# Kernel tuning notes

Hardware: AMD Instinct MI355X
Metric: run time of the kernel (lower is better)

The kernel has to match this reference:

```python
import jax, jax.numpy as jnp
import numpy as np

C = 128  # n_filters; input channels must equal n_filters due to residual


def setup_inputs() -> dict:
    key = jax.random.key(0)
    kx, kw = jax.random.split(key)
    x = jax.random.normal(kx, (8, 64, 512, C), dtype=jnp.float32)
    # 1x1 conv, no bias == dense over channel axis: [C, 2C]
    W_qkv = jax.random.normal(kw, (C, 2 * C), dtype=jnp.float32) * (1.0 / np.sqrt(C))
    return {"x": x, "W_qkv": W_qkv}


def reference(x, W_qkv):
    # qkv: [B,H,W,2C]; split -> qk [B,H,W,C] -> q,k [B,H,W,C/2]; v [B,H,W,C]
    qkv = jnp.einsum('bhwc,cd->bhwd', x, W_qkv)
    half = C // 2
    q = qkv[..., :half]
    k = qkv[..., half:C]
    v = qkv[..., C:]
    # scores over the W (time) axis; NOTE: original applies no 1/sqrt(d) scaling
    scores = jnp.einsum('bhqc,bhkc->bhqk', q, k)  # [B,H,W,W]
    w = jax.nn.softmax(scores, axis=-1)
    y = jnp.einsum('bhqk,bhkc->bhqc', w, v)  # [B,H,W,C]
    y = x + y  # with_skip_connection=True
    return (y, w)
```

## Files before the change

### kernel.cpp

```cpp
#include <hip/hip_runtime.h>
#include <hip/hip_bf16.h>

typedef short s16x8 __attribute__((ext_vector_type(8)));
typedef float f32x4 __attribute__((ext_vector_type(4)));

#define MFMA_BF16(a,b,c) __builtin_amdgcn_mfma_f32_16x16x32_bf16((a),(b),(c),0,0,0)

static __device__ __forceinline__ unsigned short f2bf(float f){
  unsigned u = __builtin_bit_cast(unsigned, f);
  u += 0x7fffu + ((u >> 16) & 1u);
  return (unsigned short)(u >> 16);
}
static __device__ __forceinline__ float bf2f(unsigned short h){
  unsigned u = ((unsigned)h) << 16;
  return __builtin_bit_cast(float, u);
}
static __device__ __forceinline__ int swzi(int row, int col, int lw){
  const int chunk = (col >> 3) ^ ((row ^ (row >> 3)) & 7);
  return row*lw + (chunk << 3) + (col & 7);
}

__global__ __launch_bounds__(128) void k0_wt(const float* __restrict__ W,
                                             unsigned short* __restrict__ wtH,
                                             unsigned short* __restrict__ wtL){
  const int n = blockIdx.x;
  const int c = threadIdx.x;
  const float v = W[(size_t)c*256 + n];
  const unsigned short h = f2bf(v);
  wtH[n*128 + c] = h;
  wtL[n*128 + c] = f2bf(v - bf2f(h));
}

__global__ __launch_bounds__(512,2) void k1_qkv(const float* __restrict__ x,
    const unsigned short* __restrict__ wtH, const unsigned short* __restrict__ wtL,
    unsigned short* __restrict__ qh, unsigned short* __restrict__ ql,
    unsigned short* __restrict__ kh, unsigned short* __restrict__ kl,
    unsigned short* __restrict__ vT){
  __shared__ unsigned short xh[16384], xl[16384];
  const int t = threadIdx.x;
  const int lane = t & 63, wid = t >> 6;
  const int li = lane & 15, g = lane >> 4;
  const int m0 = blockIdx.x * 128;
  const int wm = wid >> 2, wn = wid & 3;

  {
    const int row = t >> 2, cb = (t & 3) * 32;
    const float* src = x + (size_t)(m0 + row)*128 + cb;
    #pragma unroll
    for (int gg = 0; gg < 4; ++gg){
      const float4 v0 = ((const float4*)src)[2*gg];
      const float4 v1 = ((const float4*)src)[2*gg + 1];
      const float vv[8] = {v0.x,v0.y,v0.z,v0.w,v1.x,v1.y,v1.z,v1.w};
      s16x8 h, l;
      #pragma unroll
      for (int j = 0; j < 8; ++j){
        const unsigned short hb = f2bf(vv[j]);
        h[j] = (short)hb;
        l[j] = (short)f2bf(vv[j] - bf2f(hb));
      }
      const int idx = swzi(row, cb + 8*gg, 128);
      *(s16x8*)&xh[idx] = h;
      *(s16x8*)&xl[idx] = l;
    }
  }
  __syncthreads();

  {
    f32x4 acc[4][2] = {};
    #pragma unroll
    for (int ks = 0; ks < 4; ++ks){
      const int col = ks*32 + g*8;
      s16x8 ah[4], al[4];
      #pragma unroll
      for (int mi = 0; mi < 4; ++mi){
        const int idx = swzi(wm*64 + mi*16 + li, col, 128);
        ah[mi] = *(const s16x8*)&xh[idx];
        al[mi] = *(const s16x8*)&xl[idx];
      }
      #pragma unroll
      for (int ni = 0; ni < 2; ++ni){
        const size_t boff = (size_t)(wn*32 + ni*16 + li)*128 + col;
        const s16x8 bh = *(const s16x8*)(wtH + boff);
        const s16x8 bl = *(const s16x8*)(wtL + boff);
        #pragma unroll
        for (int mi = 0; mi < 4; ++mi){
          acc[mi][ni] = MFMA_BF16(bh, ah[mi], acc[mi][ni]);
          acc[mi][ni] = MFMA_BF16(bh, al[mi], acc[mi][ni]);
          acc[mi][ni] = MFMA_BF16(bl, ah[mi], acc[mi][ni]);
        }
      }
    }
    #pragma unroll
    for (int mi = 0; mi < 4; ++mi)
      #pragma unroll
      for (int ni = 0; ni < 2; ++ni){
        const int pos = m0 + wm*64 + mi*16 + li;
        const int och = wn*32 + ni*16 + g*4;
        ushort4 hv, lv;
        #pragma unroll
        for (int r = 0; r < 4; ++r){
          const float v = acc[mi][ni][r];
          const unsigned short hb = f2bf(v);
          ((unsigned short*)&hv)[r] = hb;
          ((unsigned short*)&lv)[r] = f2bf(v - bf2f(hb));
        }
        const size_t off = (size_t)pos*64 + (och & 63);
        if (wn < 2){ *(ushort4*)&qh[off] = hv; *(ushort4*)&ql[off] = lv; }
        else       { *(ushort4*)&kh[off] = hv; *(ushort4*)&kl[off] = lv; }
      }
  }

  {
    f32x4 acc[4][2] = {};
    #pragma unroll
    for (int ks = 0; ks < 4; ++ks){
      const int col = ks*32 + g*8;
      s16x8 ah[4], al[4];
      #pragma unroll
      for (int mi = 0; mi < 4; ++mi){
        const int idx = swzi(wm*64 + mi*16 + li, col, 128);
        ah[mi] = *(const s16x8*)&xh[idx];
        al[mi] = *(const s16x8*)&xl[idx];
      }
      #pragma unroll
      for (int ni = 0; ni < 2; ++ni){
        const size_t boff = (size_t)(128 + wn*32 + ni*16 + li)*128 + col;
        const s16x8 bh = *(const s16x8*)(wtH + boff);
        const s16x8 bl = *(const s16x8*)(wtL + boff);
        #pragma unroll
        for (int mi = 0; mi < 4; ++mi){
          acc[mi][ni] = MFMA_BF16(ah[mi], bh, acc[mi][ni]);
          acc[mi][ni] = MFMA_BF16(ah[mi], bl, acc[mi][ni]);
          acc[mi][ni] = MFMA_BF16(al[mi], bh, acc[mi][ni]);
        }
      }
    }
    #pragma unroll
    for (int mi = 0; mi < 4; ++mi)
      #pragma unroll
      for (int ni = 0; ni < 2; ++ni){
        const int growb = m0 + wm*64 + mi*16 + g*4;
        const int ch = wn*32 + ni*16 + li;
        const int head = growb >> 9, posb = growb & 511;
        ushort4 pv;
        #pragma unroll
        for (int r = 0; r < 4; ++r)
          ((unsigned short*)&pv)[r] = f2bf(acc[mi][ni][r]);
        *(ushort4*)&vT[((size_t)head << 16) + ch*512 + posb] = pv;
      }
  }
}

__global__ __launch_bounds__(512,2) void k2_attn(
    const unsigned short* __restrict__ qh, const unsigned short* __restrict__ ql,
    const unsigned short* __restrict__ kh, const unsigned short* __restrict__ kl,
    const unsigned short* __restrict__ vT, const float* __restrict__ x,
    float* __restrict__ y, float* __restrict__ wout){
  __shared__ unsigned short wlds[32768];
  __shared__ float redm[512], reds[512];

  const int t = threadIdx.x;
  const int lane = t & 63, wid = t >> 6;
  const int li = lane & 15, g = lane >> 4;
  const int bi = blockIdx.x;
  const int head = (bi & 7) + 8 * (bi >> 6);
  const int qt = (bi >> 3) & 7;
  const size_t hbase = (size_t)head * 512;
  const int q0 = qt * 64;
  const int kbase = wid * 64;

  f32x4 acc[4][4] = {};
  #pragma unroll
  for (int ks = 0; ks < 2; ++ks){
    const int col = ks*32 + g*8;
    s16x8 qbh[4], qbl[4];
    #pragma unroll
    for (int qj = 0; qj < 4; ++qj){
      const size_t aoff = (hbase + q0 + qj*16 + li)*64 + col;
      qbh[qj] = *(const s16x8*)(qh + aoff);
      qbl[qj] = *(const s16x8*)(ql + aoff);
    }
    #pragma unroll
    for (int ni = 0; ni < 4; ++ni){
      const size_t boff = (hbase + kbase + ni*16 + li)*64 + col;
      const s16x8 ah = *(const s16x8*)(kh + boff);
      const s16x8 al = *(const s16x8*)(kl + boff);
      #pragma unroll
      for (int qj = 0; qj < 4; ++qj){
        acc[qj][ni] = MFMA_BF16(ah, qbh[qj], acc[qj][ni]);
        acc[qj][ni] = MFMA_BF16(al, qbh[qj], acc[qj][ni]);
        acc[qj][ni] = MFMA_BF16(ah, qbl[qj], acc[qj][ni]);
      }
    }
  }

  float fsc[4];
  #pragma unroll
  for (int qj = 0; qj < 4; ++qj){
    float m = acc[qj][0][0];
    #pragma unroll
    for (int ni = 0; ni < 4; ++ni)
      #pragma unroll
      for (int r = 0; r < 4; ++r) m = fmaxf(m, acc[qj][ni][r]);
    m = fmaxf(m, __shfl_xor(m, 16));
    m = fmaxf(m, __shfl_xor(m, 32));
    float s = 0.f;
    #pragma unroll
    for (int ni = 0; ni < 4; ++ni)
      #pragma unroll
      for (int r = 0; r < 4; ++r){
        const float e = __expf(acc[qj][ni][r] - m);
        acc[qj][ni][r] = e;
        s += e;
      }
    s += __shfl_xor(s, 16);
    s += __shfl_xor(s, 32);
    if (g == 0){
      redm[(qj*16 + li)*8 + wid] = m;
      reds[(qj*16 + li)*8 + wid] = s;
    }
    fsc[qj] = m;
  }
  __syncthreads();
  #pragma unroll
  for (int qj = 0; qj < 4; ++qj){
    const int row = qj*16 + li;
    const f32x4 m0v = *(const f32x4*)&redm[row*8];
    const f32x4 m1v = *(const f32x4*)&redm[row*8 + 4];
    const f32x4 s0v = *(const f32x4*)&reds[row*8];
    const f32x4 s1v = *(const f32x4*)&reds[row*8 + 4];
    float M = fmaxf(fmaxf(fmaxf(m0v[0], m0v[1]), fmaxf(m0v[2], m0v[3])),
                    fmaxf(fmaxf(m1v[0], m1v[1]), fmaxf(m1v[2], m1v[3])));
    float S = s0v[0]*__expf(m0v[0] - M) + s0v[1]*__expf(m0v[1] - M)
            + s0v[2]*__expf(m0v[2] - M) + s0v[3]*__expf(m0v[3] - M)
            + s1v[0]*__expf(m1v[0] - M) + s1v[1]*__expf(m1v[1] - M)
            + s1v[2]*__expf(m1v[2] - M) + s1v[3]*__expf(m1v[3] - M);
    fsc[qj] = __expf(fsc[qj] - M) / S;
  }

  #pragma unroll
  for (int qj = 0; qj < 4; ++qj){
    const int row = qj*16 + li;
    float* wrow = wout + (hbase + q0 + row)*512;
    #pragma unroll
    for (int ni = 0; ni < 4; ++ni){
      const int col = kbase + ni*16 + g*4;
      f32x4 wv;
      ushort4 pv;
      #pragma unroll
      for (int r = 0; r < 4; ++r){
        const float v = acc[qj][ni][r] * fsc[qj];
        wv[r] = v;
        ((unsigned short*)&pv)[r] = f2bf(v);
      }
      *(f32x4*)&wrow[col] = wv;
      *(ushort4*)&wlds[swzi(row, col, 512)] = pv;
    }
  }
  __syncthreads();

  const int c0 = wid * 16;
  f32x4 yacc[4] = {};
  const unsigned short* vhead = vT + ((size_t)head << 16) + (size_t)(c0 + li)*512;
  #pragma unroll
  for (int kt = 0; kt < 16; ++kt){
    const int kp0 = kt*32 + g*8;
    const s16x8 vb = *(const s16x8*)&vhead[kp0];
    #pragma unroll
    for (int mi = 0; mi < 4; ++mi){
      const s16x8 aw = *(const s16x8*)&wlds[swzi(mi*16 + li, kp0, 512)];
      yacc[mi] = MFMA_BF16(vb, aw, yacc[mi]);
    }
  }

  #pragma unroll
  for (int mi = 0; mi < 4; ++mi){
    const int row = mi*16 + li;
    const size_t idx = (hbase + q0 + row)*128 + c0 + g*4;
    const f32x4 xv = __builtin_nontemporal_load((const f32x4*)&x[idx]);
    f32x4 ov;
    ov[0] = xv[0] + yacc[mi][0];
    ov[1] = xv[1] + yacc[mi][1];
    ov[2] = xv[2] + yacc[mi][2];
    ov[3] = xv[3] + yacc[mi][3];
    *(f32x4*)&y[idx] = ov;
  }
}

extern "C" void kernel_launch(void* const* d_in, const int* in_sizes, int n_in,
                              void* d_out, int out_size, void* d_ws, size_t ws_size,
                              hipStream_t stream){
  (void)in_sizes; (void)n_in; (void)out_size; (void)ws_size;
  const float* x = (const float*)d_in[0];
  const float* W = (const float*)d_in[1];
  float* y    = (float*)d_out;
  float* wout = y + (size_t)33554432;

  char* ws = (char*)d_ws;
  unsigned short* qh  = (unsigned short*)(ws);
  unsigned short* ql  = (unsigned short*)(ws +  33554432ull);
  unsigned short* kh  = (unsigned short*)(ws +  67108864ull);
  unsigned short* kl  = (unsigned short*)(ws + 100663296ull);
  unsigned short* vT  = (unsigned short*)(ws + 134217728ull);
  unsigned short* wtH = (unsigned short*)(ws + 201326592ull);
  unsigned short* wtL = (unsigned short*)(ws + 201392128ull);

  hipLaunchKernelGGL(k0_wt,   dim3(256),  dim3(128), 0, stream, W, wtH, wtL);
  hipLaunchKernelGGL(k1_qkv,  dim3(2048), dim3(512), 0, stream, x, wtH, wtL,
                     qh, ql, kh, kl, vT);
  hipLaunchKernelGGL(k2_attn, dim3(4096), dim3(512), 0, stream,
                     qh, ql, kh, kl, vT, x, y, wout);
}
```

Before: 518.4 us.

## Fuse QKV projection and attention into one per-head kernel

Merges the QKV projection kernel and the attention kernel into a single kernel with one block per head. Each block first computes Q/K/V for its 512 positions in four chunks, then loops over eight query tiles to compute softmax and the output. This removes one launch and aims to keep the per-head Q/K/V in cache between the two phases. The grid shrinks from 4096 blocks to 512 and each block's work becomes serial, which reduces parallelism and latency hiding. The Q/K/V written by other threads are read back from global memory after only a block-level fence.

```diff
diff --git a/kernel.cpp b/kernel.cpp
--- a/kernel.cpp
+++ b/kernel.cpp
@@ -31,259 +31,260 @@
   wtL[n*128 + c] = f2bf(v - bf2f(h));
 }
 
-__global__ __launch_bounds__(512,2) void k1_qkv(const float* __restrict__ x,
+__global__ __launch_bounds__(512,2) void kf(const float* __restrict__ x,
     const unsigned short* __restrict__ wtH, const unsigned short* __restrict__ wtL,
     unsigned short* __restrict__ qh, unsigned short* __restrict__ ql,
     unsigned short* __restrict__ kh, unsigned short* __restrict__ kl,
-    unsigned short* __restrict__ vT){
-  __shared__ unsigned short xh[16384], xl[16384];
+    unsigned short* __restrict__ vT,
+    float* __restrict__ y, float* __restrict__ wout){
+  __shared__ __align__(16) unsigned short smem[34816];
+  unsigned short* xh   = smem;
+  unsigned short* xl   = smem + 16384;
+  unsigned short* wlds = smem;
+  float* redm = (float*)(smem + 32768);
+  float* reds = redm + 512;
+
   const int t = threadIdx.x;
   const int lane = t & 63, wid = t >> 6;
   const int li = lane & 15, g = lane >> 4;
-  const int m0 = blockIdx.x * 128;
+  const int head = blockIdx.x;
+  const size_t hbase = (size_t)head * 512;
+
   const int wm = wid >> 2, wn = wid & 3;
-
-  {
-    const int row = t >> 2, cb = (t & 3) * 32;
-    const float* src = x + (size_t)(m0 + row)*128 + cb;
-    #pragma unroll
-    for (int gg = 0; gg < 4; ++gg){
-      const float4 v0 = ((const float4*)src)[2*gg];
-      const float4 v1 = ((const float4*)src)[2*gg + 1];
-      const float vv[8] = {v0.x,v0.y,v0.z,v0.w,v1.x,v1.y,v1.z,v1.w};
-      s16x8 h, l;
-      #pragma unroll
-      for (int j = 0; j < 8; ++j){
-        const unsigned short hb = f2bf(vv[j]);
-        h[j] = (short)hb;
-        l[j] = (short)f2bf(vv[j] - bf2f(hb));
-      }
-      const int idx = swzi(row, cb + 8*gg, 128);
-      *(s16x8*)&xh[idx] = h;
-      *(s16x8*)&xl[idx] = l;
+  for (int rc = 0; rc < 4; ++rc){
+    const int m0 = head*512 + rc*128;
+    if (rc) __syncthreads();
+    {
+      const int row = t >> 2, cb = (t & 3) * 32;
+      const float* src = x + (size_t)(m0 + row)*128 + cb;
+      #pragma unroll
+      for (int gg = 0; gg < 4; ++gg){
+        const float4 v0 = ((const float4*)src)[2*gg];
+        const float4 v1 = ((const float4*)src)[2*gg + 1];
+        const float vv[8] = {v0.x,v0.y,v0.z,v0.w,v1.x,v1.y,v1.z,v1.w};
+        s16x8 h, l;
+        #pragma unroll
+        for (int j = 0; j < 8; ++j){
+          const unsigned short hb = f2bf(vv[j]);
+          h[j] = (short)hb;
+          l[j] = (short)f2bf(vv[j] - bf2f(hb));
+        }
+        const int idx = swzi(row, cb + 8*gg, 128);
+        *(s16x8*)&xh[idx] = h;
+        *(s16x8*)&xl[idx] = l;
+      }
+    }
+    __syncthreads();
+
+    {
+      f32x4 acc[4][2] = {};
+      #pragma unroll
+      for (int ks = 0; ks < 4; ++ks){
+        const int col = ks*32 + g*8;
+        s16x8 ah[4], al[4];
+        #pragma unroll
+        for (int mi = 0; mi < 4; ++mi){
+          const int idx = swzi(wm*64 + mi*16 + li, col, 128);
+          ah[mi] = *(const s16x8*)&xh[idx];
+          al[mi] = *(const s16x8*)&xl[idx];
+        }
+        #pragma unroll
+        for (int ni = 0; ni < 2; ++ni){
+          const size_t boff = (size_t)(wn*32 + ni*16 + li)*128 + col;
+          const s16x8 bh = *(const s16x8*)(wtH + boff);
+          const s16x8 bl = *(const s16x8*)(wtL + boff);
+          #pragma unroll
+          for (int mi = 0; mi < 4; ++mi){
+            acc[mi][ni] = MFMA_BF16(bh, ah[mi], acc[mi][ni]);
+            acc[mi][ni] = MFMA_BF16(bh, al[mi], acc[mi][ni]);
+            acc[mi][ni] = MFMA_BF16(bl, ah[mi], acc[mi][ni]);
+          }
+        }
+      }
+      #pragma unroll
+      for (int mi = 0; mi < 4; ++mi)
+        #pragma unroll
+        for (int ni = 0; ni < 2; ++ni){
+          const int pos = m0 + wm*64 + mi*16 + li;
+          const int och = wn*32 + ni*16 + g*4;
+          ushort4 hv, lv;
+          #pragma unroll
+          for (int r = 0; r < 4; ++r){
+            const float v = acc[mi][ni][r];
+            const unsigned short hb = f2bf(v);
+            ((unsigned short*)&hv)[r] = hb;
+            ((unsigned short*)&lv)[r] = f2bf(v - bf2f(hb));
+          }
+          const size_t off = (size_t)pos*64 + (och & 63);
+          if (wn < 2){ *(ushort4*)&qh[off] = hv; *(ushort4*)&ql[off] = lv; }
+          else       { *(ushort4*)&kh[off] = hv; *(ushort4*)&kl[off] = lv; }
+        }
+    }
+
+    {
+      f32x4 acc[4][2] = {};
+      #pragma unroll
+      for (int ks = 0; ks < 4; ++ks){
+        const int col = ks*32 + g*8;
+        s16x8 ah[4], al[4];
+        #pragma unroll
+        for (int mi = 0; mi < 4; ++mi){
+          const int idx = swzi(wm*64 + mi*16 + li, col, 128);
+          ah[mi] = *(const s16x8*)&xh[idx];
+          al[mi] = *(const s16x8*)&xl[idx];
+        }
+        #pragma unroll
+        for (int ni = 0; ni < 2; ++ni){
+          const size_t boff = (size_t)(128 + wn*32 + ni*16 + li)*128 + col;
+          const s16x8 bh = *(const s16x8*)(wtH + boff);
+          const s16x8 bl = *(const s16x8*)(wtL + boff);
+          #pragma unroll
+          for (int mi = 0; mi < 4; ++mi){
+            acc[mi][ni] = MFMA_BF16(ah[mi], bh, acc[mi][ni]);
+            acc[mi][ni] = MFMA_BF16(ah[mi], bl, acc[mi][ni]);
+            acc[mi][ni] = MFMA_BF16(al[mi], bh, acc[mi][ni]);
+          }
+        }
+      }
+      #pragma unroll
+      for (int mi = 0; mi < 4; ++mi)
+        #pragma unroll
+        for (int ni = 0; ni < 2; ++ni){
+          const int growb = m0 + wm*64 + mi*16 + g*4;
+          const int ch = wn*32 + ni*16 + li;
+          const int posb = growb & 511;
+          ushort4 pv;
+          #pragma unroll
+          for (int r = 0; r < 4; ++r)
+            ((unsigned short*)&pv)[r] = f2bf(acc[mi][ni][r]);
+          *(ushort4*)&vT[((size_t)head << 16) + ch*512 + posb] = pv;
+        }
     }
   }
+
+  __threadfence_block();
   __syncthreads();
 
-  {
-    f32x4 acc[4][2] = {};
-    #pragma unroll
-    for (int ks = 0; ks < 4; ++ks){
+  const int kbase = wid * 64;
+  for (int qt = 0; qt < 8; ++qt){
+    const int q0 = qt * 64;
+
+    f32x4 acc[4][4] = {};
+    #pragma unroll
+    for (int ks = 0; ks < 2; ++ks){
       const int col = ks*32 + g*8;
-      s16x8 ah[4], al[4];
+      s16x8 qbh[4], qbl[4];
+      #pragma unroll
+      for (int qj = 0; qj < 4; ++qj){
+        const size_t aoff = (hbase + q0 + qj*16 + li)*64 + col;
+        qbh[qj] = *(const s16x8*)(qh + aoff);
+        qbl[qj] = *(const s16x8*)(ql + aoff);
+      }
+      #pragma unroll
+      for (int ni = 0; ni < 4; ++ni){
+        const size_t boff = (hbase + kbase + ni*16 + li)*64 + col;
+        const s16x8 ah = *(const s16x8*)(kh + boff);
+        const s16x8 al = *(const s16x8*)(kl + boff);
+        #pragma unroll
+        for (int qj = 0; qj < 4; ++qj){
+          acc[qj][ni] = MFMA_BF16(ah, qbh[qj], acc[qj][ni]);
+          acc[qj][ni] = MFMA_BF16(al, qbh[qj], acc[qj][ni]);
+          acc[qj][ni] = MFMA_BF16(ah, qbl[qj], acc[qj][ni]);
+        }
+      }
+    }
+
+    float fsc[4];
+    #pragma unroll
+    for (int qj = 0; qj < 4; ++qj){
+      float m = acc[qj][0][0];
+      #pragma unroll
+      for (int ni = 0; ni < 4; ++ni)
+        #pragma unroll
+        for (int r = 0; r < 4; ++r) m = fmaxf(m, acc[qj][ni][r]);
+      m = fmaxf(m, __shfl_xor(m, 16));
+      m = fmaxf(m, __shfl_xor(m, 32));
+      float s = 0.f;
+      #pragma unroll
+      for (int ni = 0; ni < 4; ++ni)
+        #pragma unroll
+        for (int r = 0; r < 4; ++r){
+          const float e = __expf(acc[qj][ni][r] - m);
+          acc[qj][ni][r] = e;
+          s += e;
+        }
+      s += __shfl_xor(s, 16);
+      s += __shfl_xor(s, 32);
+      if (g == 0){
+        redm[(qj*16 + li)*8 + wid] = m;
+        reds[(qj*16 + li)*8 + wid] = s;
+      }
+      fsc[qj] = m;
+    }
+    __syncthreads();
+    #pragma unroll
+    for (int qj = 0; qj < 4; ++qj){
+      const int row = qj*16 + li;
+      const f32x4 m0v = *(const f32x4*)&redm[row*8];
+      const f32x4 m1v = *(const f32x4*)&redm[row*8 + 4];
+      const f32x4 s0v = *(const f32x4*)&reds[row*8];
+      const f32x4 s1v = *(const f32x4*)&reds[row*8 + 4];
+      float M = fmaxf(fmaxf(fmaxf(m0v[0], m0v[1]), fmaxf(m0v[2], m0v[3])),
+                      fmaxf(fmaxf(m1v[0], m1v[1]), fmaxf(m1v[2], m1v[3])));
+      float S = s0v[0]*__expf(m0v[0] - M) + s0v[1]*__expf(m0v[1] - M)
+              + s0v[2]*__expf(m0v[2] - M) + s0v[3]*__expf(m0v[3] - M)
+              + s1v[0]*__expf(m1v[0] - M) + s1v[1]*__expf(m1v[1] - M)
+              + s1v[2]*__expf(m1v[2] - M) + s1v[3]*__expf(m1v[3] - M);
+      fsc[qj] = __expf(fsc[qj] - M) / S;
+    }
+
+    #pragma unroll
+    for (int qj = 0; qj < 4; ++qj){
+      const int row = qj*16 + li;
+      float* wrow = wout + (hbase + q0 + row)*512;
+      #pragma unroll
+      for (int ni = 0; ni < 4; ++ni){
+        const int col = kbase + ni*16 + g*4;
+        f32x4 wv;
+        ushort4 pv;
+        #pragma unroll
+        for (int r = 0; r < 4; ++r){
+          const float v = acc[qj][ni][r] * fsc[qj];
+          wv[r] = v;
+          ((unsigned short*)&pv)[r] = f2bf(v);
+        }
+        *(f32x4*)&wrow[col] = wv;
+        *(ushort4*)&wlds[swzi(row, col, 512)] = pv;
+      }
+    }
+    __syncthreads();
+
+    const int c0 = wid * 16;
+    f32x4 yacc[4] = {};
+    const unsigned short* vhead = vT + ((size_t)head << 16) + (size_t)(c0 + li)*512;
+    #pragma unroll
+    for (int kt = 0; kt < 16; ++kt){
+      const int kp0 = kt*32 + g*8;
+      const s16x8 vb = *(const s16x8*)&vhead[kp0];
       #pragma unroll
       for (int mi = 0; mi < 4; ++mi){
-        const int idx = swzi(wm*64 + mi*16 + li, col, 128);
-        ah[mi] = *(const s16x8*)&xh[idx];
-        al[mi] = *(const s16x8*)&xl[idx];
-      }
-      #pragma unroll
-      for (int ni = 0; ni < 2; ++ni){
-        const size_t boff = (size_t)(wn*32 + ni*16 + li)*128 + col;
-        const s16x8 bh = *(const s16x8*)(wtH + boff);
-        const s16x8 bl = *(const s16x8*)(wtL + boff);
-        #pragma unroll
-        for (int mi = 0; mi < 4; ++mi){
-          acc[mi][ni] = MFMA_BF16(bh, ah[mi], acc[mi][ni]);
-          acc[mi][ni] = MFMA_BF16(bh, al[mi], acc[mi][ni]);
-          acc[mi][ni] = MFMA_BF16(bl, ah[mi], acc[mi][ni]);
-        }
-      }
-    }
-    #pragma unroll
-    for (int mi = 0; mi < 4; ++mi)
-      #pragma unroll
-      for (int ni = 0; ni < 2; ++ni){
-        const int pos = m0 + wm*64 + mi*16 + li;
-        const int och = wn*32 + ni*16 + g*4;
-        ushort4 hv, lv;
-        #pragma unroll
-        for (int r = 0; r < 4; ++r){
-          const float v = acc[mi][ni][r];
-          const unsigned short hb = f2bf(v);
-          ((unsigned short*)&hv)[r] = hb;
-          ((unsigned short*)&lv)[r] = f2bf(v - bf2f(hb));
-        }
-        const size_t off = (size_t)pos*64 + (och & 63);
-        if (wn < 2){ *(ushort4*)&qh[off] = hv; *(ushort4*)&ql[off] = lv; }
-        else       { *(ushort4*)&kh[off] = hv; *(ushort4*)&kl[off] = lv; }
-      }
-  }
-
-  {
-    f32x4 acc[4][2] = {};
-    #pragma unroll
-    for (int ks = 0; ks < 4; ++ks){
-      const int col = ks*32 + g*8;
-      s16x8 ah[4], al[4];
-      #pragma unroll
-      for (int mi = 0; mi < 4; ++mi){
-        const int idx = swzi(wm*64 + mi*16 + li, col, 128);
-        ah[mi] = *(const s16x8*)&xh[idx];
-        al[mi] = *(const s16x8*)&xl[idx];
-      }
-      #pragma unroll
-      for (int ni = 0; ni < 2; ++ni){
-        const size_t boff = (size_t)(128 + wn*32 + ni*16 + li)*128 + col;
-        const s16x8 bh = *(const s16x8*)(wtH + boff);
-        const s16x8 bl = *(const s16x8*)(wtL + boff);
-        #pragma unroll
-        for (int mi = 0; mi < 4; ++mi){
-          acc[mi][ni] = MFMA_BF16(ah[mi], bh, acc[mi][ni]);
-          acc[mi][ni] = MFMA_BF16(ah[mi], bl, acc[mi][ni]);
-          acc[mi][ni] = MFMA_BF16(al[mi], bh, acc[mi][ni]);
-        }
-      }
-    }
-    #pragma unroll
-    for (int mi = 0; mi < 4; ++mi)
-      #pragma unroll
-      for (int ni = 0; ni < 2; ++ni){
-        const int growb = m0 + wm*64 + mi*16 + g*4;
-        const int ch = wn*32 + ni*16 + li;
-        const int head = growb >> 9, posb = growb & 511;
-        ushort4 pv;
-        #pragma unroll
-        for (int r = 0; r < 4; ++r)
-          ((unsigned short*)&pv)[r] = f2bf(acc[mi][ni][r]);
-        *(ushort4*)&vT[((size_t)head << 16) + ch*512 + posb] = pv;
-      }
-  }
-}
-
-__global__ __launch_bounds__(512,2) void k2_attn(
-    const unsigned short* __restrict__ qh, const unsigned short* __restrict__ ql,
-    const unsigned short* __restrict__ kh, const unsigned short* __restrict__ kl,
-    const unsigned short* __restrict__ vT, const float* __restrict__ x,
-    float* __restrict__ y, float* __restrict__ wout){
-  __shared__ unsigned short wlds[32768];
-  __shared__ float redm[512], reds[512];
-
-  const int t = threadIdx.x;
-  const int lane = t & 63, wid = t >> 6;
-  const int li = lane & 15, g = lane >> 4;
-  const int bi = blockIdx.x;
-  const int head = (bi & 7) + 8 * (bi >> 6);
-  const int qt = (bi >> 3) & 7;
-  const size_t hbase = (size_t)head * 512;
-  const int q0 = qt * 64;
-  const int kbase = wid * 64;
-
-  f32x4 acc[4][4] = {};
-  #pragma unroll
-  for (int ks = 0; ks < 2; ++ks){
-    const int col = ks*32 + g*8;
-    s16x8 qbh[4], qbl[4];
-    #pragma unroll
-    for (int qj = 0; qj < 4; ++qj){
-      const size_t aoff = (hbase + q0 + qj*16 + li)*64 + col;
-      qbh[qj] = *(const s16x8*)(qh + aoff);
-      qbl[qj] = *(const s16x8*)(ql + aoff);
-    }
-    #pragma unroll
-    for (int ni = 0; ni < 4; ++ni){
-      const size_t boff = (hbase + kbase + ni*16 + li)*64 + col;
-      const s16x8 ah = *(const s16x8*)(kh + boff);
-      const s16x8 al = *(const s16x8*)(kl + boff);
-      #pragma unroll
-      for (int qj = 0; qj < 4; ++qj){
-        acc[qj][ni] = MFMA_BF16(ah, qbh[qj], acc[qj][ni]);
-        acc[qj][ni] = MFMA_BF16(al, qbh[qj], acc[qj][ni]);
-        acc[qj][ni] = MFMA_BF16(ah, qbl[qj], acc[qj][ni]);
-      }
-    }
-  }
-
-  float fsc[4];
-  #pragma unroll
-  for (int qj = 0; qj < 4; ++qj){
-    float m = acc[qj][0][0];
-    #pragma unroll
-    for (int ni = 0; ni < 4; ++ni)
-      #pragma unroll
-      for (int r = 0; r < 4; ++r) m = fmaxf(m, acc[qj][ni][r]);
-    m = fmaxf(m, __shfl_xor(m, 16));
-    m = fmaxf(m, __shfl_xor(m, 32));
-    float s = 0.f;
-    #pragma unroll
-    for (int ni = 0; ni < 4; ++ni)
-      #pragma unroll
-      for (int r = 0; r < 4; ++r){
-        const float e = __expf(acc[qj][ni][r] - m);
-        acc[qj][ni][r] = e;
-        s += e;
-      }
-    s += __shfl_xor(s, 16);
-    s += __shfl_xor(s, 32);
-    if (g == 0){
-      redm[(qj*16 + li)*8 + wid] = m;
-      reds[(qj*16 + li)*8 + wid] = s;
-    }
-    fsc[qj] = m;
-  }
-  __syncthreads();
-  #pragma unroll
-  for (int qj = 0; qj < 4; ++qj){
-    const int row = qj*16 + li;
-    const f32x4 m0v = *(const f32x4*)&redm[row*8];
-    const f32x4 m1v = *(const f32x4*)&redm[row*8 + 4];
-    const f32x4 s0v = *(const f32x4*)&reds[row*8];
-    const f32x4 s1v = *(const f32x4*)&reds[row*8 + 4];
-    float M = fmaxf(fmaxf(fmaxf(m0v[0], m0v[1]), fmaxf(m0v[2], m0v[3])),
-                    fmaxf(fmaxf(m1v[0], m1v[1]), fmaxf(m1v[2], m1v[3])));
-    float S = s0v[0]*__expf(m0v[0] - M) + s0v[1]*__expf(m0v[1] - M)
-            + s0v[2]*__expf(m0v[2] - M) + s0v[3]*__expf(m0v[3] - M)
-            + s1v[0]*__expf(m1v[0] - M) + s1v[1]*__expf(m1v[1] - M)
-            + s1v[2]*__expf(m1v[2] - M) + s1v[3]*__expf(m1v[3] - M);
-    fsc[qj] = __expf(fsc[qj] - M) / S;
-  }
-
-  #pragma unroll
-  for (int qj = 0; qj < 4; ++qj){
-    const int row = qj*16 + li;
-    float* wrow = wout + (hbase + q0 + row)*512;
-    #pragma unroll
-    for (int ni = 0; ni < 4; ++ni){
-      const int col = kbase + ni*16 + g*4;
-      f32x4 wv;
-      ushort4 pv;
-      #pragma unroll
-      for (int r = 0; r < 4; ++r){
-        const float v = acc[qj][ni][r] * fsc[qj];
-        wv[r] = v;
-        ((unsigned short*)&pv)[r] = f2bf(v);
-      }
-      *(f32x4*)&wrow[col] = wv;
-      *(ushort4*)&wlds[swzi(row, col, 512)] = pv;
-    }
-  }
-  __syncthreads();
-
-  const int c0 = wid * 16;
-  f32x4 yacc[4] = {};
-  const unsigned short* vhead = vT + ((size_t)head << 16) + (size_t)(c0 + li)*512;
-  #pragma unroll
-  for (int kt = 0; kt < 16; ++kt){
-    const int kp0 = kt*32 + g*8;
-    const s16x8 vb = *(const s16x8*)&vhead[kp0];
+        const s16x8 aw = *(const s16x8*)&wlds[swzi(mi*16 + li, kp0, 512)];
+        yacc[mi] = MFMA_BF16(vb, aw, yacc[mi]);
+      }
+    }
+
     #pragma unroll
     for (int mi = 0; mi < 4; ++mi){
-      const s16x8 aw = *(const s16x8*)&wlds[swzi(mi*16 + li, kp0, 512)];
-      yacc[mi] = MFMA_BF16(vb, aw, yacc[mi]);
-    }
-  }
-
-  #pragma unroll
-  for (int mi = 0; mi < 4; ++mi){
-    const int row = mi*16 + li;
-    const size_t idx = (hbase + q0 + row)*128 + c0 + g*4;
-    const f32x4 xv = __builtin_nontemporal_load((const f32x4*)&x[idx]);
-    f32x4 ov;
-    ov[0] = xv[0] + yacc[mi][0];
-    ov[1] = xv[1] + yacc[mi][1];
-    ov[2] = xv[2] + yacc[mi][2];
-    ov[3] = xv[3] + yacc[mi][3];
-    *(f32x4*)&y[idx] = ov;
+      const int row = mi*16 + li;
+      const size_t idx = (hbase + q0 + row)*128 + c0 + g*4;
+      const f32x4 xv = __builtin_nontemporal_load((const f32x4*)&x[idx]);
+      f32x4 ov;
+      ov[0] = xv[0] + yacc[mi][0];
+      ov[1] = xv[1] + yacc[mi][1];
+      ov[2] = xv[2] + yacc[mi][2];
+      ov[3] = xv[3] + yacc[mi][3];
+      *(f32x4*)&y[idx] = ov;
+    }
   }
 }
 
@@ -305,9 +306,7 @@
   unsigned short* wtH = (unsigned short*)(ws + 201326592ull);
   unsigned short* wtL = (unsigned short*)(ws + 201392128ull);
 
-  hipLaunchKernelGGL(k0_wt,   dim3(256),  dim3(128), 0, stream, W, wtH, wtL);
-  hipLaunchKernelGGL(k1_qkv,  dim3(2048), dim3(512), 0, stream, x, wtH, wtL,
-                     qh, ql, kh, kl, vT);
-  hipLaunchKernelGGL(k2_attn, dim3(4096), dim3(512), 0, stream,
-                     qh, ql, kh, kl, vT, x, y, wout);
-}
+  hipLaunchKernelGGL(k0_wt, dim3(256), dim3(128), 0, stream, W, wtH, wtL);
+  hipLaunchKernelGGL(kf,    dim3(512), dim3(512), 0, stream, x, wtH, wtL,
+                     qh, ql, kh, kl, vT, y, wout);
+}
```

Measured after the change: 505.1 us. -2.6%, faster.

## Process all query tiles per head in one block, keeping K and V in registers

Applied to the files above, without the earlier changes.

The attention kernel now launches one block per head instead of one per (head, query tile). Each block loads its K slice and the transposed V slice into registers once, then loops over the 8 query tiles, reusing them for scores and the weighted sum. This removes the repeated K/V global loads across query-tile blocks. In exchange, register use rises sharply (which may cause spills under the 512-thread, 2-blocks-per-CU bound), and the grid shrinks to 512 blocks, leaving less parallelism to hide the large output writes.

```diff
diff --git a/kernel.cpp b/kernel.cpp
--- a/kernel.cpp
+++ b/kernel.cpp
@@ -162,128 +162,140 @@
   const int t = threadIdx.x;
   const int lane = t & 63, wid = t >> 6;
   const int li = lane & 15, g = lane >> 4;
-  const int bi = blockIdx.x;
-  const int head = (bi & 7) + 8 * (bi >> 6);
-  const int qt = (bi >> 3) & 7;
+  const int head = blockIdx.x;
   const size_t hbase = (size_t)head * 512;
-  const int q0 = qt * 64;
   const int kbase = wid * 64;
 
-  f32x4 acc[4][4] = {};
+  s16x8 kregh[2][4], kregl[2][4];
   #pragma unroll
-  for (int ks = 0; ks < 2; ++ks){
-    const int col = ks*32 + g*8;
-    s16x8 qbh[4], qbl[4];
+  for (int ks = 0; ks < 2; ++ks)
+    #pragma unroll
+    for (int ni = 0; ni < 4; ++ni){
+      const size_t boff = (hbase + kbase + ni*16 + li)*64 + ks*32 + g*8;
+      kregh[ks][ni] = *(const s16x8*)(kh + boff);
+      kregl[ks][ni] = *(const s16x8*)(kl + boff);
+    }
+  s16x8 vreg[16];
+  {
+    const unsigned short* vhead = vT + ((size_t)head << 16) + (size_t)(wid*16 + li)*512;
+    #pragma unroll
+    for (int kt = 0; kt < 16; ++kt)
+      vreg[kt] = *(const s16x8*)&vhead[kt*32 + g*8];
+  }
+
+  for (int qt = 0; qt < 8; ++qt){
+    const int q0 = qt * 64;
+
+    f32x4 acc[4][4] = {};
+    #pragma unroll
+    for (int ks = 0; ks < 2; ++ks){
+      const int col = ks*32 + g*8;
+      s16x8 qbh[4], qbl[4];
+      #pragma unroll
+      for (int qj = 0; qj < 4; ++qj){
+        const size_t aoff = (hbase + q0 + qj*16 + li)*64 + col;
+        qbh[qj] = *(const s16x8*)(qh + aoff);
+        qbl[qj] = *(const s16x8*)(ql + aoff);
+      }
+      #pragma unroll
+      for (int ni = 0; ni < 4; ++ni)
+        #pragma unroll
+        for (int qj = 0; qj < 4; ++qj){
+          acc[qj][ni] = MFMA_BF16(kregh[ks][ni], qbh[qj], acc[qj][ni]);
+          acc[qj][ni] = MFMA_BF16(kregl[ks][ni], qbh[qj], acc[qj][ni]);
+          acc[qj][ni] = MFMA_BF16(kregh[ks][ni], qbl[qj], acc[qj][ni]);
+        }
+    }
+
+    float fsc[4];
     #pragma unroll
     for (int qj = 0; qj < 4; ++qj){
-      const size_t aoff = (hbase + q0 + qj*16 + li)*64 + col;
-      qbh[qj] = *(const s16x8*)(qh + aoff);
-      qbl[qj] = *(const s16x8*)(ql + aoff);
-    }
-    #pragma unroll
-    for (int ni = 0; ni < 4; ++ni){
-      const size_t boff = (hbase + kbase + ni*16 + li)*64 + col;
-      const s16x8 ah = *(const s16x8*)(kh + boff);
-      const s16x8 al = *(const s16x8*)(kl + boff);
-      #pragma unroll
-      for (int qj = 0; qj < 4; ++qj){
-        acc[qj][ni] = MFMA_BF16(ah, qbh[qj], acc[qj][ni]);
-        acc[qj][ni] = MFMA_BF16(al, qbh[qj], acc[qj][ni]);
-        acc[qj][ni] = MFMA_BF16(ah, qbl[qj], acc[qj][ni]);
-      }
-    }
-  }
-
-  float fsc[4];
-  #pragma unroll
-  for (int qj = 0; qj < 4; ++qj){
-    float m = acc[qj][0][0];
-    #pragma unroll
-    for (int ni = 0; ni < 4; ++ni)
-      #pragma unroll
-      for (int r = 0; r < 4; ++r) m = fmaxf(m, acc[qj][ni][r]);
-    m = fmaxf(m, __shfl_xor(m, 16));
-    m = fmaxf(m, __shfl_xor(m, 32));
-    float s = 0.f;
-    #pragma unroll
-    for (int ni = 0; ni < 4; ++ni)
-      #pragma unroll
-      for (int r = 0; r < 4; ++r){
-        const float e = __expf(acc[qj][ni][r] - m);
-        acc[qj][ni][r] = e;
-        s += e;
-      }
-    s += __shfl_xor(s, 16);
-    s += __shfl_xor(s, 32);
-    if (g == 0){
-      redm[(qj*16 + li)*8 + wid] = m;
-      reds[(qj*16 + li)*8 + wid] = s;
-    }
-    fsc[qj] = m;
-  }
-  __syncthreads();
-  #pragma unroll
-  for (int qj = 0; qj < 4; ++qj){
-    const int row = qj*16 + li;
-    const f32x4 m0v = *(const f32x4*)&redm[row*8];
-    const f32x4 m1v = *(const f32x4*)&redm[row*8 + 4];
-    const f32x4 s0v = *(const f32x4*)&reds[row*8];
-    const f32x4 s1v = *(const f32x4*)&reds[row*8 + 4];
-    float M = fmaxf(fmaxf(fmaxf(m0v[0], m0v[1]), fmaxf(m0v[2], m0v[3])),
-                    fmaxf(fmaxf(m1v[0], m1v[1]), fmaxf(m1v[2], m1v[3])));
-    float S = s0v[0]*__expf(m0v[0] - M) + s0v[1]*__expf(m0v[1] - M)
-            + s0v[2]*__expf(m0v[2] - M) + s0v[3]*__expf(m0v[3] - M)
-            + s1v[0]*__expf(m1v[0] - M) + s1v[1]*__expf(m1v[1] - M)
-            + s1v[2]*__expf(m1v[2] - M) + s1v[3]*__expf(m1v[3] - M);
-    fsc[qj] = __expf(fsc[qj] - M) / S;
-  }
-
-  #pragma unroll
-  for (int qj = 0; qj < 4; ++qj){
-    const int row = qj*16 + li;
-    float* wrow = wout + (hbase + q0 + row)*512;
-    #pragma unroll
-    for (int ni = 0; ni < 4; ++ni){
-      const int col = kbase + ni*16 + g*4;
-      f32x4 wv;
-      ushort4 pv;
-      #pragma unroll
-      for (int r = 0; r < 4; ++r){
-        const float v = acc[qj][ni][r] * fsc[qj];
-        wv[r] = v;
-        ((unsigned short*)&pv)[r] = f2bf(v);
-      }
-      *(f32x4*)&wrow[col] = wv;
-      *(ushort4*)&wlds[swzi(row, col, 512)] = pv;
-    }
-  }
-  __syncthreads();
-
-  const int c0 = wid * 16;
-  f32x4 yacc[4] = {};
-  const unsigned short* vhead = vT + ((size_t)head << 16) + (size_t)(c0 + li)*512;
-  #pragma unroll
-  for (int kt = 0; kt < 16; ++kt){
-    const int kp0 = kt*32 + g*8;
-    const s16x8 vb = *(const s16x8*)&vhead[kp0];
+      float m = acc[qj][0][0];
+      #pragma unroll
+      for (int ni = 0; ni < 4; ++ni)
+        #pragma unroll
+        for (int r = 0; r < 4; ++r) m = fmaxf(m, acc[qj][ni][r]);
+      m = fmaxf(m, __shfl_xor(m, 16));
+      m = fmaxf(m, __shfl_xor(m, 32));
+      float s = 0.f;
+      #pragma unroll
+      for (int ni = 0; ni < 4; ++ni)
+        #pragma unroll
+        for (int r = 0; r < 4; ++r){
+          const float e = __expf(acc[qj][ni][r] - m);
+          acc[qj][ni][r] = e;
+          s += e;
+        }
+      s += __shfl_xor(s, 16);
+      s += __shfl_xor(s, 32);
+      if (g == 0){
+        redm[(qj*16 + li)*8 + wid] = m;
+        reds[(qj*16 + li)*8 + wid] = s;
+      }
+      fsc[qj] = m;
+    }
+    __syncthreads();
+    #pragma unroll
+    for (int qj = 0; qj < 4; ++qj){
+      const int row = qj*16 + li;
+      const f32x4 m0v = *(const f32x4*)&redm[row*8];
+      const f32x4 m1v = *(const f32x4*)&redm[row*8 + 4];
+      const f32x4 s0v = *(const f32x4*)&reds[row*8];
+      const f32x4 s1v = *(const f32x4*)&reds[row*8 + 4];
+      float M = fmaxf(fmaxf(fmaxf(m0v[0], m0v[1]), fmaxf(m0v[2], m0v[3])),
+                      fmaxf(fmaxf(m1v[0], m1v[1]), fmaxf(m1v[2], m1v[3])));
+      float S = s0v[0]*__expf(m0v[0] - M) + s0v[1]*__expf(m0v[1] - M)
+              + s0v[2]*__expf(m0v[2] - M) + s0v[3]*__expf(m0v[3] - M)
+              + s1v[0]*__expf(m1v[0] - M) + s1v[1]*__expf(m1v[1] - M)
+              + s1v[2]*__expf(m1v[2] - M) + s1v[3]*__expf(m1v[3] - M);
+      fsc[qj] = __expf(fsc[qj] - M) / S;
+    }
+
+    #pragma unroll
+    for (int qj = 0; qj < 4; ++qj){
+      const int row = qj*16 + li;
+      float* wrow = wout + (hbase + q0 + row)*512;
+      #pragma unroll
+      for (int ni = 0; ni < 4; ++ni){
+        const int col = kbase + ni*16 + g*4;
+        f32x4 wv;
+        ushort4 pv;
+        #pragma unroll
+        for (int r = 0; r < 4; ++r){
+          const float v = acc[qj][ni][r] * fsc[qj];
+          wv[r] = v;
+          ((unsigned short*)&pv)[r] = f2bf(v);
+        }
+        *(f32x4*)&wrow[col] = wv;
+        *(ushort4*)&wlds[swzi(row, col, 512)] = pv;
+      }
+    }
+    __syncthreads();
+
+    const int c0 = wid * 16;
+    f32x4 yacc[4] = {};
+    #pragma unroll
+    for (int kt = 0; kt < 16; ++kt){
+      const int kp0 = kt*32 + g*8;
+      #pragma unroll
+      for (int mi = 0; mi < 4; ++mi){
+        const s16x8 aw = *(const s16x8*)&wlds[swzi(mi*16 + li, kp0, 512)];
+        yacc[mi] = MFMA_BF16(vreg[kt], aw, yacc[mi]);
+      }
+    }
+
     #pragma unroll
     for (int mi = 0; mi < 4; ++mi){
-      const s16x8 aw = *(const s16x8*)&wlds[swzi(mi*16 + li, kp0, 512)];
-      yacc[mi] = MFMA_BF16(vb, aw, yacc[mi]);
-    }
-  }
-
-  #pragma unroll
-  for (int mi = 0; mi < 4; ++mi){
-    const int row = mi*16 + li;
-    const size_t idx = (hbase + q0 + row)*128 + c0 + g*4;
-    const f32x4 xv = __builtin_nontemporal_load((const f32x4*)&x[idx]);
-    f32x4 ov;
-    ov[0] = xv[0] + yacc[mi][0];
-    ov[1] = xv[1] + yacc[mi][1];
-    ov[2] = xv[2] + yacc[mi][2];
-    ov[3] = xv[3] + yacc[mi][3];
-    *(f32x4*)&y[idx] = ov;
+      const int row = mi*16 + li;
+      const size_t idx = (hbase + q0 + row)*128 + c0 + g*4;
+      const f32x4 xv = __builtin_nontemporal_load((const f32x4*)&x[idx]);
+      f32x4 ov;
+      ov[0] = xv[0] + yacc[mi][0];
+      ov[1] = xv[1] + yacc[mi][1];
+      ov[2] = xv[2] + yacc[mi][2];
+      ov[3] = xv[3] + yacc[mi][3];
+      *(f32x4*)&y[idx] = ov;
+    }
   }
 }
 
@@ -308,6 +320,6 @@
   hipLaunchKernelGGL(k0_wt,   dim3(256),  dim3(128), 0, stream, W, wtH, wtL);
   hipLaunchKernelGGL(k1_qkv,  dim3(2048), dim3(512), 0, stream, x, wtH, wtL,
                      qh, ql, kh, kl, vT);
-  hipLaunchKernelGGL(k2_attn, dim3(4096), dim3(512), 0, stream,
+  hipLaunchKernelGGL(k2_attn, dim3(512),  dim3(512), 0, stream,
                      qh, ql, kh, kl, vT, x, y, wout);
 }
```

After: 745.6 us. 43.8% more time.
